# Kernel tuning notes

Measured on AMD Instinct MI355X. Metric: run time of the kernel, lower is better.

## Reference

```python
import jax, jax.numpy as jnp
import numpy as np

B, S, E, H = 4, 2048, 1024, 16
HD = E // H  # head_dim = 64


def setup_inputs() -> dict:
    key = jax.random.key(0)
    ks = jax.random.split(key, 9)
    s_in = 1.0 / np.sqrt(E)
    return {
        "x": jax.random.normal(ks[0], (B, S, E), dtype=jnp.float32),
        "Wq": jax.random.normal(ks[1], (E, E), dtype=jnp.float32) * s_in,
        "bq": jax.random.normal(ks[2], (E,), dtype=jnp.float32) * 0.01,
        "Wk": jax.random.normal(ks[3], (E, E), dtype=jnp.float32) * s_in,
        "bk": jax.random.normal(ks[4], (E,), dtype=jnp.float32) * 0.01,
        "Wv": jax.random.normal(ks[5], (E, E), dtype=jnp.float32) * s_in,
        "bv": jax.random.normal(ks[6], (E,), dtype=jnp.float32) * 0.01,
        "Wo": jax.random.normal(ks[7], (E, E), dtype=jnp.float32) * s_in,
        "bo": jax.random.normal(ks[8], (E,), dtype=jnp.float32) * 0.01,
    }


def reference(x, Wq, bq, Wk, bk, Wv, bv, Wo, bo):
    b, s, e = x.shape
    # fused QKV projections (equivalent to concatenated per-head linears)
    q = x @ Wq + bq  # [b, s, e]
    k = x @ Wk + bk
    v = x @ Wv + bv
    # split heads: [b, h, s, hd]
    def split(t):
        return t.reshape(b, s, H, HD).transpose(0, 2, 1, 3)
    q, k, v = split(q), split(k), split(v)
    scale = 1.0 / np.sqrt(HD)
    attn = jnp.einsum("bhqd,bhkd->bhqk", q, k) * scale  # [b, h, s, s]
    causal = jnp.tril(jnp.ones((s, s), dtype=bool))
    attn = jnp.where(causal[None, None], attn, -jnp.inf)
    attn = jax.nn.softmax(attn, axis=-1)
    y = jnp.einsum("bhqk,bhkd->bhqd", attn, v)  # [b, h, s, hd]
    y = y.transpose(0, 2, 1, 3).reshape(b, s, e)
    return y @ Wo + bo
```

## Files before the change

kernel.cpp:

```cpp
#include <hip/hip_runtime.h>
#include <hip/hip_bf16.h>

#define B_ 4
#define S_ 2048
#define E_ 1024
#define H_ 16
#define HD_ 64
#define QS 3072

typedef __attribute__((ext_vector_type(8))) short bf16x8;
typedef __attribute__((ext_vector_type(4))) float f32x4;

__device__ __forceinline__ float b2f(unsigned short u) {
    union { unsigned u; float f; } v; v.u = ((unsigned)u) << 16; return v.f;
}
__device__ __forceinline__ unsigned short f2b(float f) {
    union { float f; unsigned u; } v; v.f = f;
    unsigned lsb = (v.u >> 16) & 1u;
    v.u += 0x7fffu + lsb;
    return (unsigned short)(v.u >> 16);
}
__device__ __forceinline__ unsigned cvtpk_bf16(float lo, float hi) {
    unsigned r;
    asm("v_cvt_pk_bf16_f32 %0, %1, %2" : "=v"(r) : "v"(lo), "v"(hi));
    return r;
}

typedef const __attribute__((address_space(1))) unsigned glb_u32;
typedef __attribute__((address_space(3))) unsigned lds_u32;
__device__ __forceinline__ void gl_lds16(const unsigned short* g,
                                         unsigned short* l) {
    __builtin_amdgcn_global_load_lds((glb_u32*)g, (lds_u32*)l, 16, 0, 0);
}

__global__ void cvt_f32_to_bf16(const float* __restrict__ in,
                                unsigned short* __restrict__ out, int n8) {
    int i = blockIdx.x * blockDim.x + threadIdx.x;
    if (i >= n8) return;
    const float4* p = (const float4*)(in + (size_t)i * 8);
    float4 a = p[0], b = p[1];
    bf16x8 o;
    o[0] = (short)f2b(a.x); o[1] = (short)f2b(a.y);
    o[2] = (short)f2b(a.z); o[3] = (short)f2b(a.w);
    o[4] = (short)f2b(b.x); o[5] = (short)f2b(b.y);
    o[6] = (short)f2b(b.z); o[7] = (short)f2b(b.w);
    *(bf16x8*)(out + (size_t)i * 8) = o;
}

__global__ void transpose_cvt(const float* __restrict__ W,
                              unsigned short* __restrict__ Wt) {
    __shared__ float tile[32][33];
    int tx = threadIdx.x, ty = threadIdx.y;
    int x0 = blockIdx.x * 32, y0 = blockIdx.y * 32;
#pragma unroll
    for (int j = 0; j < 32; j += 8)
        tile[ty + j][tx] = W[(size_t)(y0 + ty + j) * E_ + x0 + tx];
    __syncthreads();
#pragma unroll
    for (int j = 0; j < 32; j += 8)
        Wt[(size_t)(x0 + ty + j) * E_ + y0 + tx] = f2b(tile[tx][ty + j]);
}

#define BM 128
#define BN 128
#define BK 32

__global__ __launch_bounds__(256) void gemm_bt(
        const unsigned short* __restrict__ A,
        const unsigned short* __restrict__ Bt,
        const float* __restrict__ b0, const float* __restrict__ b1,
        const float* __restrict__ b2,
        unsigned short* __restrict__ Cb,
        int M, int N, int K) {
    __shared__ unsigned short As[BM][BK];
    __shared__ unsigned short Bs[BN][BK];
    int t = threadIdx.x;
    int lane = t & 63, wid = t >> 6;
    int wr = wid >> 1, wc = wid & 1;
    int bx = blockIdx.x, by = blockIdx.y;
    const int row = t >> 2, kc = (t & 3) << 3;
    const unsigned short* ga0 = A + (size_t)(by * BM + row) * K + kc;
    const unsigned short* gb0 = Bt + (size_t)(bx * BN + row) * K + kc;
    unsigned short* la0 = &As[0][0] + (size_t)t * 8;
    unsigned short* lb0 = &Bs[0][0] + (size_t)t * 8;
    const size_t step64 = (size_t)64 * K;

    f32x4 acc[4][4] = {};

    for (int ko = 0; ko < K; ko += BK) {
        gl_lds16(ga0 + ko, la0);
        gl_lds16(ga0 + ko + step64, la0 + 2048);
        gl_lds16(gb0 + ko, lb0);
        gl_lds16(gb0 + ko + step64, lb0 + 2048);
        __syncthreads();
        int kg = (lane >> 4) << 3;
        bf16x8 af[4], bfr[4];
#pragma unroll
        for (int i = 0; i < 4; ++i) {
            af[i]  = *(const bf16x8*)&As[wr * 64 + i * 16 + (lane & 15)][kg];
            bfr[i] = *(const bf16x8*)&Bs[wc * 64 + i * 16 + (lane & 15)][kg];
        }
#pragma unroll
        for (int i = 0; i < 4; ++i)
#pragma unroll
            for (int j = 0; j < 4; ++j)
                acc[i][j] = __builtin_amdgcn_mfma_f32_16x16x32_bf16(
                    af[i], bfr[j], acc[i][j], 0, 0, 0);
        __syncthreads();
    }

#pragma unroll
    for (int i = 0; i < 4; ++i) {
        int row0 = by * BM + wr * 64 + i * 16 + ((lane >> 4) << 2);
#pragma unroll
        for (int j = 0; j < 4; ++j) {
            int col = bx * BN + wc * 64 + j * 16 + (lane & 15);
            const float* bp = (col < 1024) ? b0 : ((col < 2048) ? b1 : b2);
            float bv = bp[col & 1023];
#pragma unroll
            for (int r = 0; r < 4; ++r) {
                int rr = row0 + r;
                Cb[(size_t)rr * N + col] = f2b(acc[i][j][r] + bv);
            }
        }
    }
}

__global__ __launch_bounds__(256) void gemm_bt_out(
        const unsigned short* __restrict__ A,
        const unsigned short* __restrict__ Bt,
        const float* __restrict__ bias,
        float* __restrict__ Cf, int M, int N, int K) {
    __shared__ unsigned short As[64][BK];
    __shared__ unsigned short Bs[BN][BK];
    int t = threadIdx.x;
    int lane = t & 63, wid = t >> 6;
    int wr = wid >> 1, wc = wid & 1;
    int bx = blockIdx.x, by = blockIdx.y;
    const int row = t >> 2, kc = (t & 3) << 3;
    const unsigned short* ga0 = A + (size_t)(by * 64 + row) * K + kc;
    const unsigned short* gb0 = Bt + (size_t)(bx * BN + row) * K + kc;
    unsigned short* la0 = &As[0][0] + (size_t)t * 8;
    unsigned short* lb0 = &Bs[0][0] + (size_t)t * 8;
    const size_t step64 = (size_t)64 * K;

    f32x4 acc[2][4] = {};

    for (int ko = 0; ko < K; ko += BK) {
        gl_lds16(ga0 + ko, la0);
        gl_lds16(gb0 + ko, lb0);
        gl_lds16(gb0 + ko + step64, lb0 + 2048);
        __syncthreads();
        int kg = (lane >> 4) << 3;
        bf16x8 af[2], bfr[4];
#pragma unroll
        for (int i = 0; i < 2; ++i)
            af[i] = *(const bf16x8*)&As[wr * 32 + i * 16 + (lane & 15)][kg];
#pragma unroll
        for (int j = 0; j < 4; ++j)
            bfr[j] = *(const bf16x8*)&Bs[wc * 64 + j * 16 + (lane & 15)][kg];
#pragma unroll
        for (int i = 0; i < 2; ++i)
#pragma unroll
            for (int j = 0; j < 4; ++j)
                acc[i][j] = __builtin_amdgcn_mfma_f32_16x16x32_bf16(
                    af[i], bfr[j], acc[i][j], 0, 0, 0);
        __syncthreads();
    }

#pragma unroll
    for (int i = 0; i < 2; ++i) {
        int row0 = by * 64 + wr * 32 + i * 16 + ((lane >> 4) << 2);
#pragma unroll
        for (int j = 0; j < 4; ++j) {
            int col = bx * BN + wc * 64 + j * 16 + (lane & 15);
            float bv = bias[col];
#pragma unroll
            for (int r = 0; r < 4; ++r)
                Cf[(size_t)(row0 + r) * N + col] = acc[i][j][r] + bv;
        }
    }
}

#define KVBLK 64

__global__ __launch_bounds__(256) void attn_mfma(
        const unsigned short* __restrict__ QKV,
        unsigned short* __restrict__ Yb) {
    __shared__ unsigned short Ks[2][KVBLK][64];
    __shared__ unsigned short Vt[2][64][KVBLK];
    __shared__ unsigned short Pl[4][16][64];

    int t = threadIdx.x;
    int lane = t & 63, wid = t >> 6;
    int l15 = lane & 15, lg = lane >> 4;
    int bh = blockIdx.x;
    int b = bh >> 4, h = bh & 15;
    int by = gridDim.y - 1 - blockIdx.y;
    int qbase = by * 128 + wid * 32;
    int vidx = lg << 4;

    const int kk1 = t >> 3, kk2 = 32 + kk1;
    const int kg1 = ((t & 7) ^ (kk1 & 7)) << 3;
    const int kg2 = ((t & 7) ^ (kk2 & 7)) << 3;
    const int vkey = t >> 2, vc4 = (t & 3) << 4;

    const unsigned short* kvbase = QKV + ((size_t)b * S_) * QS + 1024 + h * 64;

    const float qscale = 0.125f * 1.44269504f;
    bf16x8 qf[2][2];
#pragma unroll
    for (int mt = 0; mt < 2; ++mt)
#pragma unroll
        for (int ks = 0; ks < 2; ++ks) {
            int row = qbase + mt * 16 + l15;
            bf16x8 v = *(const bf16x8*)&QKV[((size_t)(b * S_ + row)) * QS +
                                            h * 64 + ks * 32 + lg * 8];
#pragma unroll
            for (int e = 0; e < 8; ++e)
                qf[mt][ks][e] = (short)f2b(b2f((unsigned short)v[e]) * qscale);
        }

    f32x4 yacc[2][4] = {};
    float m_[2] = {-1e30f, -1e30f}, l_[2] = {0.f, 0.f};

    int ntiles = by * 2 + 2;

    {
        gl_lds16(kvbase + (size_t)kk1 * QS + kg1, &Ks[0][0][0] + (size_t)t * 8);
        gl_lds16(kvbase + (size_t)kk2 * QS + kg2,
                 &Ks[0][0][0] + 2048 + (size_t)t * 8);
        const unsigned short* vsrc = kvbase + 1024 + (size_t)vkey * QS + vc4;
        bf16x8 v0 = *(const bf16x8*)vsrc;
        bf16x8 v1 = *(const bf16x8*)(vsrc + 8);
#pragma unroll
        for (int e = 0; e < 8; ++e) {
            int d0 = vc4 + e, d1 = vc4 + 8 + e;
            int s0 = (d0 & 7) ^ ((d0 >> 3) & 7);
            int s1 = (d1 & 7) ^ ((d1 >> 3) & 7);
            Vt[0][d0][vkey ^ (s0 << 3)] = (unsigned short)v0[e];
            Vt[0][d1][vkey ^ (s1 << 3)] = (unsigned short)v1[e];
        }
    }
    __syncthreads();

    int cur = 0;
    for (int kt = 0; kt < ntiles; ++kt) {
        int k0 = kt * KVBLK;
        bool pre = (kt + 1 < ntiles);
        bf16x8 nv0, nv1;
        if (pre) {
            const unsigned short* kb = kvbase + (size_t)(k0 + KVBLK) * QS;
            unsigned short* ld = &Ks[cur ^ 1][0][0];
            gl_lds16(kb + (size_t)kk1 * QS + kg1, ld + (size_t)t * 8);
            gl_lds16(kb + (size_t)kk2 * QS + kg2, ld + 2048 + (size_t)t * 8);
            const unsigned short* vsrc =
                kb + 1024 + (size_t)vkey * QS + vc4;
            nv0 = *(const bf16x8*)vsrc;
            nv1 = *(const bf16x8*)(vsrc + 8);
        }

        if (k0 <= qbase + 31) {
            bool boundary = (k0 + KVBLK - 1 > qbase);
            f32x4 sacc[2][4] = {};
#pragma unroll
            for (int ks = 0; ks < 2; ++ks) {
                bf16x8 kf[4];
#pragma unroll
                for (int n = 0; n < 4; ++n)
                    kf[n] = *(const bf16x8*)&Ks[cur][n * 16 + l15]
                              [(ks * 32 + lg * 8) ^ ((l15 & 7) << 3)];
#pragma unroll
                for (int mt = 0; mt < 2; ++mt)
#pragma unroll
                    for (int n = 0; n < 4; ++n)
                        sacc[mt][n] = __builtin_amdgcn_mfma_f32_16x16x32_bf16(
                            kf[n], qf[mt][ks], sacc[mt][n], 0, 0, 0);
            }

#pragma unroll
            for (int mt = 0; mt < 2; ++mt) {
                int qv = qbase + mt * 16 + l15;
                if (boundary) {
#pragma unroll
                    for (int n = 0; n < 4; ++n)
#pragma unroll
                        for (int r = 0; r < 4; ++r)
                            if (k0 + n * 16 + lg * 4 + r > qv)
                                sacc[mt][n][r] = -3e38f;
                }
                float pm = -3e38f;
#pragma unroll
                for (int n = 0; n < 4; ++n)
#pragma unroll
                    for (int r = 0; r < 4; ++r)
                        pm = fmaxf(pm, sacc[mt][n][r]);
                pm = fmaxf(pm, __shfl_xor(pm, 16));
                pm = fmaxf(pm, __shfl_xor(pm, 32));
                float mo = m_[mt];
                float mn = mo;
                bool need = __any(pm > mo + 8.0f);
                if (need) {
                    mn = fmaxf(mo, pm);
                    float corr = __builtin_exp2f(mo - mn);
                    m_[mt] = mn;
                    l_[mt] *= corr;
                    int ci = __float_as_int(corr);
#pragma unroll
                    for (int r = 0; r < 4; ++r) {
                        float cq = __int_as_float(
                            __builtin_amdgcn_ds_bpermute(vidx + 4 * r, ci));
#pragma unroll
                        for (int n = 0; n < 4; ++n) yacc[mt][n][r] *= cq;
                    }
                }
                float rs = 0.f;
#pragma unroll
                for (int n = 0; n < 4; ++n)
#pragma unroll
                    for (int r = 0; r < 4; ++r) {
                        float p = __builtin_exp2f(sacc[mt][n][r] - mn);
                        sacc[mt][n][r] = p;
                        rs += p;
                    }
                rs += __shfl_xor(rs, 16);
                rs += __shfl_xor(rs, 32);
                l_[mt] += rs;
#pragma unroll
                for (int n = 0; n < 4; ++n)
#pragma unroll
                    for (int j = 0; j < 2; ++j) {
                        unsigned u = cvtpk_bf16(sacc[mt][n][2 * j],
                                                sacc[mt][n][2 * j + 1]);
                        int col = (n * 16 + lg * 4 + 2 * j) ^ ((l15 & 7) << 3);
                        *(unsigned*)&Pl[wid][l15][col] = u;
                    }
#pragma unroll
                for (int ks = 0; ks < 2; ++ks) {
                    bf16x8 pa, vf[4];
                    pa = *(const bf16x8*)&Pl[wid][l15]
                           [(ks * 32 + lg * 8) ^ ((l15 & 7) << 3)];
#pragma unroll
                    for (int nd = 0; nd < 4; ++nd) {
                        int d = nd * 16 + l15;
                        int sig = (d & 7) ^ ((d >> 3) & 7);
                        vf[nd] = *(const bf16x8*)&Vt[cur][d]
                                   [(ks * 32 + lg * 8) ^ (sig << 3)];
                    }
#pragma unroll
                    for (int nd = 0; nd < 4; ++nd)
                        yacc[mt][nd] = __builtin_amdgcn_mfma_f32_16x16x32_bf16(
                            pa, vf[nd], yacc[mt][nd], 0, 0, 0);
                }
            }
        }

        if (pre) {
#pragma unroll
            for (int e = 0; e < 8; ++e) {
                int d0 = vc4 + e, d1 = vc4 + 8 + e;
                int s0 = (d0 & 7) ^ ((d0 >> 3) & 7);
                int s1 = (d1 & 7) ^ ((d1 >> 3) & 7);
                Vt[cur ^ 1][d0][vkey ^ (s0 << 3)] = (unsigned short)nv0[e];
                Vt[cur ^ 1][d1][vkey ^ (s1 << 3)] = (unsigned short)nv1[e];
            }
        }
        __syncthreads();
        cur ^= 1;
    }

#pragma unroll
    for (int mt = 0; mt < 2; ++mt) {
        float inv = 1.f / l_[mt];
        int ii = __float_as_int(inv);
        float iv[4];
#pragma unroll
        for (int r = 0; r < 4; ++r)
            iv[r] = __int_as_float(
                __builtin_amdgcn_ds_bpermute(vidx + 4 * r, ii));
#pragma unroll
        for (int n = 0; n < 4; ++n)
#pragma unroll
            for (int r = 0; r < 4; ++r) {
                int row = qbase + mt * 16 + lg * 4 + r;
                int d = n * 16 + l15;
                Yb[((size_t)(b * S_ + row)) * E_ + h * 64 + d] =
                    f2b(yacc[mt][n][r] * iv[r]);
            }
    }
}

extern "C" void kernel_launch(void* const* d_in, const int* in_sizes, int n_in,
                              void* d_out, int out_size, void* d_ws, size_t ws_size,
                              hipStream_t stream) {
    const float* x  = (const float*)d_in[0];
    const float* Wq = (const float*)d_in[1];
    const float* bq = (const float*)d_in[2];
    const float* Wk = (const float*)d_in[3];
    const float* bk = (const float*)d_in[4];
    const float* Wv = (const float*)d_in[5];
    const float* bv = (const float*)d_in[6];
    const float* Wo = (const float*)d_in[7];
    const float* bo = (const float*)d_in[8];

    char* ws = (char*)d_ws;
    const size_t M = (size_t)B_ * S_;
    unsigned short* xb   = (unsigned short*)ws;
    unsigned short* QKVb = (unsigned short*)(ws + (16ull << 20));
    unsigned short* Wqkv = (unsigned short*)(ws + (64ull << 20));
    unsigned short* Wto  = (unsigned short*)(ws + (70ull << 20));
    unsigned short* Yb   = xb;

    int n8 = (int)(M * E_ / 8);
    cvt_f32_to_bf16<<<(n8 + 255) / 256, 256, 0, stream>>>(x, xb, n8);

    dim3 tb(32, 8), tg(32, 32);
    transpose_cvt<<<tg, tb, 0, stream>>>(Wq, Wqkv);
    transpose_cvt<<<tg, tb, 0, stream>>>(Wk, Wqkv + (size_t)1024 * E_);
    transpose_cvt<<<tg, tb, 0, stream>>>(Wv, Wqkv + (size_t)2048 * E_);
    transpose_cvt<<<tg, tb, 0, stream>>>(Wo, Wto);

    dim3 gq(QS / BN, M / BM);
    gemm_bt<<<gq, 256, 0, stream>>>(xb, Wqkv, bq, bk, bv, QKVb,
                                    (int)M, QS, E_);

    dim3 ag(B_ * H_, S_ / 128);
    attn_mfma<<<ag, 256, 0, stream>>>(QKVb, Yb);

    dim3 gg(E_ / BN, M / 64);
    gemm_bt_out<<<gg, 256, 0, stream>>>(Yb, Wto, bo, (float*)d_out,
                                        (int)M, E_, E_);
}
```

Baseline: 217.6 us.

## Make attention persistent with atomic work queue and merge weight transposes

The attention kernel becomes persistent: 768 blocks take (query-tile, head) units from a global atomic counter, heaviest causal tiles first, which is meant to improve load balance across CUs. It also adds s_setprio around MFMA sections, hoists the V fragment loads ahead of the softmax, and defers the cross-lane row-sum reduction to the end of the loop. The four weight transpose launches are merged into a single 3D-grid launch. In exchange it adds a memset launch and an atomic per work unit, and the launch-bounds occupancy hint of 3 may add register pressure.

```diff
diff --git a/kernel.cpp b/kernel.cpp
--- a/kernel.cpp
+++ b/kernel.cpp
@@ -7,6 +7,7 @@
 #define H_ 16
 #define HD_ 64
 #define QS 3072
+#define NUNITS (B_ * H_ * (S_ / 128))
 
 typedef __attribute__((ext_vector_type(8))) short bf16x8;
 typedef __attribute__((ext_vector_type(4))) float f32x4;
@@ -47,9 +48,16 @@
     *(bf16x8*)(out + (size_t)i * 8) = o;
 }
 
-__global__ void transpose_cvt(const float* __restrict__ W,
-                              unsigned short* __restrict__ Wt) {
+__global__ void transpose_cvt4(const float* __restrict__ W0,
+                               const float* __restrict__ W1,
+                               const float* __restrict__ W2,
+                               const float* __restrict__ W3,
+                               unsigned short* __restrict__ Wqkv,
+                               unsigned short* __restrict__ Wto) {
     __shared__ float tile[32][33];
+    int z = blockIdx.z;
+    const float* W = (z == 0) ? W0 : (z == 1) ? W1 : (z == 2) ? W2 : W3;
+    unsigned short* Wt = (z < 3) ? Wqkv + (size_t)z * 1024 * E_ : Wto;
     int tx = threadIdx.x, ty = threadIdx.y;
     int x0 = blockIdx.x * 32, y0 = blockIdx.y * 32;
 #pragma unroll
@@ -184,209 +192,233 @@
 
 #define KVBLK 64
 
-__global__ __launch_bounds__(256) void attn_mfma(
+__global__ __launch_bounds__(256, 3) void attn_mfma(
         const unsigned short* __restrict__ QKV,
-        unsigned short* __restrict__ Yb) {
+        unsigned short* __restrict__ Yb,
+        unsigned int* __restrict__ counter) {
     __shared__ unsigned short Ks[2][KVBLK][64];
     __shared__ unsigned short Vt[2][64][KVBLK];
     __shared__ unsigned short Pl[4][16][64];
+    __shared__ unsigned int s_u;
 
     int t = threadIdx.x;
     int lane = t & 63, wid = t >> 6;
     int l15 = lane & 15, lg = lane >> 4;
-    int bh = blockIdx.x;
-    int b = bh >> 4, h = bh & 15;
-    int by = gridDim.y - 1 - blockIdx.y;
-    int qbase = by * 128 + wid * 32;
     int vidx = lg << 4;
 
     const int kk1 = t >> 3, kk2 = 32 + kk1;
     const int kg1 = ((t & 7) ^ (kk1 & 7)) << 3;
     const int kg2 = ((t & 7) ^ (kk2 & 7)) << 3;
     const int vkey = t >> 2, vc4 = (t & 3) << 4;
-
-    const unsigned short* kvbase = QKV + ((size_t)b * S_) * QS + 1024 + h * 64;
-
     const float qscale = 0.125f * 1.44269504f;
-    bf16x8 qf[2][2];
-#pragma unroll
-    for (int mt = 0; mt < 2; ++mt)
-#pragma unroll
-        for (int ks = 0; ks < 2; ++ks) {
-            int row = qbase + mt * 16 + l15;
-            bf16x8 v = *(const bf16x8*)&QKV[((size_t)(b * S_ + row)) * QS +
-                                            h * 64 + ks * 32 + lg * 8];
-#pragma unroll
-            for (int e = 0; e < 8; ++e)
-                qf[mt][ks][e] = (short)f2b(b2f((unsigned short)v[e]) * qscale);
-        }
-
-    f32x4 yacc[2][4] = {};
-    float m_[2] = {-1e30f, -1e30f}, l_[2] = {0.f, 0.f};
-
-    int ntiles = by * 2 + 2;
-
-    {
-        gl_lds16(kvbase + (size_t)kk1 * QS + kg1, &Ks[0][0][0] + (size_t)t * 8);
-        gl_lds16(kvbase + (size_t)kk2 * QS + kg2,
-                 &Ks[0][0][0] + 2048 + (size_t)t * 8);
-        const unsigned short* vsrc = kvbase + 1024 + (size_t)vkey * QS + vc4;
-        bf16x8 v0 = *(const bf16x8*)vsrc;
-        bf16x8 v1 = *(const bf16x8*)(vsrc + 8);
-#pragma unroll
-        for (int e = 0; e < 8; ++e) {
-            int d0 = vc4 + e, d1 = vc4 + 8 + e;
-            int s0 = (d0 & 7) ^ ((d0 >> 3) & 7);
-            int s1 = (d1 & 7) ^ ((d1 >> 3) & 7);
-            Vt[0][d0][vkey ^ (s0 << 3)] = (unsigned short)v0[e];
-            Vt[0][d1][vkey ^ (s1 << 3)] = (unsigned short)v1[e];
-        }
-    }
-    __syncthreads();
-
-    int cur = 0;
-    for (int kt = 0; kt < ntiles; ++kt) {
-        int k0 = kt * KVBLK;
-        bool pre = (kt + 1 < ntiles);
-        bf16x8 nv0, nv1;
-        if (pre) {
-            const unsigned short* kb = kvbase + (size_t)(k0 + KVBLK) * QS;
-            unsigned short* ld = &Ks[cur ^ 1][0][0];
-            gl_lds16(kb + (size_t)kk1 * QS + kg1, ld + (size_t)t * 8);
-            gl_lds16(kb + (size_t)kk2 * QS + kg2, ld + 2048 + (size_t)t * 8);
+
+    for (;;) {
+        __syncthreads();
+        if (t == 0) s_u = atomicAdd(counter, 1u);
+        __syncthreads();
+        unsigned u = s_u;
+        if (u >= (unsigned)NUNITS) break;
+        int qt = (S_ / 128 - 1) - (int)(u >> 6);
+        int bh = (int)(u & 63);
+        int b = bh >> 4, h = bh & 15;
+        int qbase = qt * 128 + wid * 32;
+        const unsigned short* kvbase =
+            QKV + ((size_t)b * S_) * QS + 1024 + h * 64;
+
+        bf16x8 qf[2][2];
+#pragma unroll
+        for (int mt = 0; mt < 2; ++mt)
+#pragma unroll
+            for (int ks = 0; ks < 2; ++ks) {
+                int row = qbase + mt * 16 + l15;
+                bf16x8 v = *(const bf16x8*)&QKV[((size_t)(b * S_ + row)) * QS +
+                                                h * 64 + ks * 32 + lg * 8];
+#pragma unroll
+                for (int e = 0; e < 8; ++e)
+                    qf[mt][ks][e] =
+                        (short)f2b(b2f((unsigned short)v[e]) * qscale);
+            }
+
+        f32x4 yacc[2][4] = {};
+        float m_[2] = {-1e30f, -1e30f}, l_[2] = {0.f, 0.f};
+        int ntiles = qt * 2 + 2;
+
+        {
+            gl_lds16(kvbase + (size_t)kk1 * QS + kg1,
+                     &Ks[0][0][0] + (size_t)t * 8);
+            gl_lds16(kvbase + (size_t)kk2 * QS + kg2,
+                     &Ks[0][0][0] + 2048 + (size_t)t * 8);
             const unsigned short* vsrc =
-                kb + 1024 + (size_t)vkey * QS + vc4;
-            nv0 = *(const bf16x8*)vsrc;
-            nv1 = *(const bf16x8*)(vsrc + 8);
-        }
-
-        if (k0 <= qbase + 31) {
-            bool boundary = (k0 + KVBLK - 1 > qbase);
-            f32x4 sacc[2][4] = {};
-#pragma unroll
-            for (int ks = 0; ks < 2; ++ks) {
-                bf16x8 kf[4];
-#pragma unroll
-                for (int n = 0; n < 4; ++n)
-                    kf[n] = *(const bf16x8*)&Ks[cur][n * 16 + l15]
-                              [(ks * 32 + lg * 8) ^ ((l15 & 7) << 3)];
-#pragma unroll
-                for (int mt = 0; mt < 2; ++mt)
-#pragma unroll
-                    for (int n = 0; n < 4; ++n)
-                        sacc[mt][n] = __builtin_amdgcn_mfma_f32_16x16x32_bf16(
-                            kf[n], qf[mt][ks], sacc[mt][n], 0, 0, 0);
-            }
-
-#pragma unroll
-            for (int mt = 0; mt < 2; ++mt) {
-                int qv = qbase + mt * 16 + l15;
-                if (boundary) {
-#pragma unroll
-                    for (int n = 0; n < 4; ++n)
-#pragma unroll
-                        for (int r = 0; r < 4; ++r)
-                            if (k0 + n * 16 + lg * 4 + r > qv)
-                                sacc[mt][n][r] = -3e38f;
-                }
-                float pm = -3e38f;
-#pragma unroll
-                for (int n = 0; n < 4; ++n)
-#pragma unroll
-                    for (int r = 0; r < 4; ++r)
-                        pm = fmaxf(pm, sacc[mt][n][r]);
-                pm = fmaxf(pm, __shfl_xor(pm, 16));
-                pm = fmaxf(pm, __shfl_xor(pm, 32));
-                float mo = m_[mt];
-                float mn = mo;
-                bool need = __any(pm > mo + 8.0f);
-                if (need) {
-                    mn = fmaxf(mo, pm);
-                    float corr = __builtin_exp2f(mo - mn);
-                    m_[mt] = mn;
-                    l_[mt] *= corr;
-                    int ci = __float_as_int(corr);
-#pragma unroll
-                    for (int r = 0; r < 4; ++r) {
-                        float cq = __int_as_float(
-                            __builtin_amdgcn_ds_bpermute(vidx + 4 * r, ci));
-#pragma unroll
-                        for (int n = 0; n < 4; ++n) yacc[mt][n][r] *= cq;
-                    }
-                }
-                float rs = 0.f;
-#pragma unroll
-                for (int n = 0; n < 4; ++n)
-#pragma unroll
-                    for (int r = 0; r < 4; ++r) {
-                        float p = __builtin_exp2f(sacc[mt][n][r] - mn);
-                        sacc[mt][n][r] = p;
-                        rs += p;
-                    }
-                rs += __shfl_xor(rs, 16);
-                rs += __shfl_xor(rs, 32);
-                l_[mt] += rs;
-#pragma unroll
-                for (int n = 0; n < 4; ++n)
-#pragma unroll
-                    for (int j = 0; j < 2; ++j) {
-                        unsigned u = cvtpk_bf16(sacc[mt][n][2 * j],
-                                                sacc[mt][n][2 * j + 1]);
-                        int col = (n * 16 + lg * 4 + 2 * j) ^ ((l15 & 7) << 3);
-                        *(unsigned*)&Pl[wid][l15][col] = u;
-                    }
-#pragma unroll
-                for (int ks = 0; ks < 2; ++ks) {
-                    bf16x8 pa, vf[4];
-                    pa = *(const bf16x8*)&Pl[wid][l15]
-                           [(ks * 32 + lg * 8) ^ ((l15 & 7) << 3)];
-#pragma unroll
-                    for (int nd = 0; nd < 4; ++nd) {
-                        int d = nd * 16 + l15;
-                        int sig = (d & 7) ^ ((d >> 3) & 7);
-                        vf[nd] = *(const bf16x8*)&Vt[cur][d]
-                                   [(ks * 32 + lg * 8) ^ (sig << 3)];
-                    }
-#pragma unroll
-                    for (int nd = 0; nd < 4; ++nd)
-                        yacc[mt][nd] = __builtin_amdgcn_mfma_f32_16x16x32_bf16(
-                            pa, vf[nd], yacc[mt][nd], 0, 0, 0);
-                }
-            }
-        }
-
-        if (pre) {
+                kvbase + 1024 + (size_t)vkey * QS + vc4;
+            bf16x8 v0 = *(const bf16x8*)vsrc;
+            bf16x8 v1 = *(const bf16x8*)(vsrc + 8);
 #pragma unroll
             for (int e = 0; e < 8; ++e) {
                 int d0 = vc4 + e, d1 = vc4 + 8 + e;
                 int s0 = (d0 & 7) ^ ((d0 >> 3) & 7);
                 int s1 = (d1 & 7) ^ ((d1 >> 3) & 7);
-                Vt[cur ^ 1][d0][vkey ^ (s0 << 3)] = (unsigned short)nv0[e];
-                Vt[cur ^ 1][d1][vkey ^ (s1 << 3)] = (unsigned short)nv1[e];
-            }
-        }
-        __syncthreads();
-        cur ^= 1;
-    }
-
-#pragma unroll
-    for (int mt = 0; mt < 2; ++mt) {
-        float inv = 1.f / l_[mt];
-        int ii = __float_as_int(inv);
-        float iv[4];
-#pragma unroll
-        for (int r = 0; r < 4; ++r)
-            iv[r] = __int_as_float(
-                __builtin_amdgcn_ds_bpermute(vidx + 4 * r, ii));
-#pragma unroll
-        for (int n = 0; n < 4; ++n)
-#pragma unroll
-            for (int r = 0; r < 4; ++r) {
-                int row = qbase + mt * 16 + lg * 4 + r;
-                int d = n * 16 + l15;
-                Yb[((size_t)(b * S_ + row)) * E_ + h * 64 + d] =
-                    f2b(yacc[mt][n][r] * iv[r]);
-            }
+                Vt[0][d0][vkey ^ (s0 << 3)] = (unsigned short)v0[e];
+                Vt[0][d1][vkey ^ (s1 << 3)] = (unsigned short)v1[e];
+            }
+        }
+        __syncthreads();
+
+        int cur = 0;
+        for (int kt = 0; kt < ntiles; ++kt) {
+            int k0 = kt * KVBLK;
+            bool pre = (kt + 1 < ntiles);
+            bf16x8 nv0, nv1;
+            if (pre) {
+                const unsigned short* kb = kvbase + (size_t)(k0 + KVBLK) * QS;
+                unsigned short* ld = &Ks[cur ^ 1][0][0];
+                gl_lds16(kb + (size_t)kk1 * QS + kg1, ld + (size_t)t * 8);
+                gl_lds16(kb + (size_t)kk2 * QS + kg2,
+                         ld + 2048 + (size_t)t * 8);
+                const unsigned short* vsrc =
+                    kb + 1024 + (size_t)vkey * QS + vc4;
+                nv0 = *(const bf16x8*)vsrc;
+                nv1 = *(const bf16x8*)(vsrc + 8);
+            }
+
+            if (k0 <= qbase + 31) {
+                bool boundary = (k0 + KVBLK - 1 > qbase);
+                f32x4 sacc[2][4] = {};
+                __builtin_amdgcn_s_setprio(1);
+#pragma unroll
+                for (int ks = 0; ks < 2; ++ks) {
+                    bf16x8 kf[4];
+#pragma unroll
+                    for (int n = 0; n < 4; ++n)
+                        kf[n] = *(const bf16x8*)&Ks[cur][n * 16 + l15]
+                                  [(ks * 32 + lg * 8) ^ ((l15 & 7) << 3)];
+#pragma unroll
+                    for (int mt = 0; mt < 2; ++mt)
+#pragma unroll
+                        for (int n = 0; n < 4; ++n)
+                            sacc[mt][n] =
+                                __builtin_amdgcn_mfma_f32_16x16x32_bf16(
+                                    kf[n], qf[mt][ks], sacc[mt][n], 0, 0, 0);
+                }
+                __builtin_amdgcn_s_setprio(0);
+
+                bf16x8 vf[2][4];
+#pragma unroll
+                for (int ks = 0; ks < 2; ++ks)
+#pragma unroll
+                    for (int nd = 0; nd < 4; ++nd) {
+                        int d = nd * 16 + l15;
+                        int sig = (d & 7) ^ ((d >> 3) & 7);
+                        vf[ks][nd] = *(const bf16x8*)&Vt[cur][d]
+                                       [(ks * 32 + lg * 8) ^ (sig << 3)];
+                    }
+
+#pragma unroll
+                for (int mt = 0; mt < 2; ++mt) {
+                    int qv = qbase + mt * 16 + l15;
+                    if (boundary) {
+#pragma unroll
+                        for (int n = 0; n < 4; ++n)
+#pragma unroll
+                            for (int r = 0; r < 4; ++r)
+                                if (k0 + n * 16 + lg * 4 + r > qv)
+                                    sacc[mt][n][r] = -3e38f;
+                    }
+                    float pm = -3e38f;
+#pragma unroll
+                    for (int n = 0; n < 4; ++n)
+#pragma unroll
+                        for (int r = 0; r < 4; ++r)
+                            pm = fmaxf(pm, sacc[mt][n][r]);
+                    pm = fmaxf(pm, __shfl_xor(pm, 16));
+                    pm = fmaxf(pm, __shfl_xor(pm, 32));
+                    float mo = m_[mt];
+                    float mn = mo;
+                    bool need = __any(pm > mo + 8.0f);
+                    if (need) {
+                        mn = fmaxf(mo, pm);
+                        float corr = __builtin_exp2f(mo - mn);
+                        m_[mt] = mn;
+                        l_[mt] *= corr;
+                        int ci = __float_as_int(corr);
+#pragma unroll
+                        for (int r = 0; r < 4; ++r) {
+                            float cq = __int_as_float(
+                                __builtin_amdgcn_ds_bpermute(vidx + 4 * r, ci));
+#pragma unroll
+                            for (int n = 0; n < 4; ++n) yacc[mt][n][r] *= cq;
+                        }
+                    }
+                    float rs = 0.f;
+#pragma unroll
+                    for (int n = 0; n < 4; ++n)
+#pragma unroll
+                        for (int r = 0; r < 4; ++r) {
+                            float p = __builtin_exp2f(sacc[mt][n][r] - mn);
+                            sacc[mt][n][r] = p;
+                            rs += p;
+                        }
+                    l_[mt] += rs;
+#pragma unroll
+                    for (int n = 0; n < 4; ++n)
+#pragma unroll
+                        for (int j = 0; j < 2; ++j) {
+                            unsigned pu = cvtpk_bf16(sacc[mt][n][2 * j],
+                                                     sacc[mt][n][2 * j + 1]);
+                            int col = (n * 16 + lg * 4 + 2 * j) ^
+                                      ((l15 & 7) << 3);
+                            *(unsigned*)&Pl[wid][l15][col] = pu;
+                        }
+                    __builtin_amdgcn_s_setprio(1);
+#pragma unroll
+                    for (int ks = 0; ks < 2; ++ks) {
+                        bf16x8 pa = *(const bf16x8*)&Pl[wid][l15]
+                                      [(ks * 32 + lg * 8) ^ ((l15 & 7) << 3)];
+#pragma unroll
+                        for (int nd = 0; nd < 4; ++nd)
+                            yacc[mt][nd] =
+                                __builtin_amdgcn_mfma_f32_16x16x32_bf16(
+                                    pa, vf[ks][nd], yacc[mt][nd], 0, 0, 0);
+                    }
+                    __builtin_amdgcn_s_setprio(0);
+                }
+            }
+
+            if (pre) {
+#pragma unroll
+                for (int e = 0; e < 8; ++e) {
+                    int d0 = vc4 + e, d1 = vc4 + 8 + e;
+                    int s0 = (d0 & 7) ^ ((d0 >> 3) & 7);
+                    int s1 = (d1 & 7) ^ ((d1 >> 3) & 7);
+                    Vt[cur ^ 1][d0][vkey ^ (s0 << 3)] = (unsigned short)nv0[e];
+                    Vt[cur ^ 1][d1][vkey ^ (s1 << 3)] = (unsigned short)nv1[e];
+                }
+            }
+            __syncthreads();
+            cur ^= 1;
+        }
+
+#pragma unroll
+        for (int mt = 0; mt < 2; ++mt) {
+            float lt = l_[mt];
+            lt += __shfl_xor(lt, 16);
+            lt += __shfl_xor(lt, 32);
+            float inv = 1.f / lt;
+            int ii = __float_as_int(inv);
+            float iv[4];
+#pragma unroll
+            for (int r = 0; r < 4; ++r)
+                iv[r] = __int_as_float(
+                    __builtin_amdgcn_ds_bpermute(vidx + 4 * r, ii));
+#pragma unroll
+            for (int n = 0; n < 4; ++n)
+#pragma unroll
+                for (int r = 0; r < 4; ++r) {
+                    int row = qbase + mt * 16 + lg * 4 + r;
+                    int d = n * 16 + l15;
+                    Yb[((size_t)(b * S_ + row)) * E_ + h * 64 + d] =
+                        f2b(yacc[mt][n][r] * iv[r]);
+                }
+        }
     }
 }
 
@@ -409,23 +441,21 @@
     unsigned short* QKVb = (unsigned short*)(ws + (16ull << 20));
     unsigned short* Wqkv = (unsigned short*)(ws + (64ull << 20));
     unsigned short* Wto  = (unsigned short*)(ws + (70ull << 20));
+    unsigned int*   cnt  = (unsigned int*)(ws + (72ull << 20));
     unsigned short* Yb   = xb;
 
     int n8 = (int)(M * E_ / 8);
     cvt_f32_to_bf16<<<(n8 + 255) / 256, 256, 0, stream>>>(x, xb, n8);
 
-    dim3 tb(32, 8), tg(32, 32);
-    transpose_cvt<<<tg, tb, 0, stream>>>(Wq, Wqkv);
-    transpose_cvt<<<tg, tb, 0, stream>>>(Wk, Wqkv + (size_t)1024 * E_);
-    transpose_cvt<<<tg, tb, 0, stream>>>(Wv, Wqkv + (size_t)2048 * E_);
-    transpose_cvt<<<tg, tb, 0, stream>>>(Wo, Wto);
+    dim3 tb(32, 8), tg(32, 32, 4);
+    transpose_cvt4<<<tg, tb, 0, stream>>>(Wq, Wk, Wv, Wo, Wqkv, Wto);
 
     dim3 gq(QS / BN, M / BM);
     gemm_bt<<<gq, 256, 0, stream>>>(xb, Wqkv, bq, bk, bv, QKVb,
                                     (int)M, QS, E_);
 
-    dim3 ag(B_ * H_, S_ / 128);
-    attn_mfma<<<ag, 256, 0, stream>>>(QKVb, Yb);
+    hipMemsetAsync(cnt, 0, sizeof(unsigned), stream);
+    attn_mfma<<<768, 256, 0, stream>>>(QKVb, Yb, cnt);
 
     dim3 gg(E_ / BN, M / 64);
     gemm_bt_out<<<gg, 256, 0, stream>>>(Yb, Wto, bo, (float*)d_out,
```

Measured after the change: 266.3 us. 22.4% more time.

## Merge weight transposes, add setprio around MFMAs, defer row-sum reduction

Applied to the files above, without the earlier changes.

Folds the four weight transpose-convert launches into one launch that uses blockIdx.z to pick the matrix. In the attention kernel it adds s_setprio around the MFMA blocks and sets a launch-bounds occupancy hint of 4. It also moves the cross-lane shuffle reduction of the softmax row sum out of the KV loop so it runs once at the end. These cut launch overhead and per-tile shuffle work and aim to improve wave scheduling, at the cost of possible register pressure from the occupancy hint.

```diff
diff --git a/kernel.cpp b/kernel.cpp
--- a/kernel.cpp
+++ b/kernel.cpp
@@ -47,9 +47,16 @@
     *(bf16x8*)(out + (size_t)i * 8) = o;
 }
 
-__global__ void transpose_cvt(const float* __restrict__ W,
-                              unsigned short* __restrict__ Wt) {
+__global__ void transpose_cvt4(const float* __restrict__ W0,
+                               const float* __restrict__ W1,
+                               const float* __restrict__ W2,
+                               const float* __restrict__ W3,
+                               unsigned short* __restrict__ Wqkv,
+                               unsigned short* __restrict__ Wto) {
     __shared__ float tile[32][33];
+    int z = blockIdx.z;
+    const float* W = (z == 0) ? W0 : (z == 1) ? W1 : (z == 2) ? W2 : W3;
+    unsigned short* Wt = (z < 3) ? Wqkv + (size_t)z * 1024 * E_ : Wto;
     int tx = threadIdx.x, ty = threadIdx.y;
     int x0 = blockIdx.x * 32, y0 = blockIdx.y * 32;
 #pragma unroll
@@ -184,7 +191,7 @@
 
 #define KVBLK 64
 
-__global__ __launch_bounds__(256) void attn_mfma(
+__global__ __launch_bounds__(256, 4) void attn_mfma(
         const unsigned short* __restrict__ QKV,
         unsigned short* __restrict__ Yb) {
     __shared__ unsigned short Ks[2][KVBLK][64];
@@ -263,6 +270,7 @@
         if (k0 <= qbase + 31) {
             bool boundary = (k0 + KVBLK - 1 > qbase);
             f32x4 sacc[2][4] = {};
+            __builtin_amdgcn_s_setprio(1);
 #pragma unroll
             for (int ks = 0; ks < 2; ++ks) {
                 bf16x8 kf[4];
@@ -277,6 +285,7 @@
                         sacc[mt][n] = __builtin_amdgcn_mfma_f32_16x16x32_bf16(
                             kf[n], qf[mt][ks], sacc[mt][n], 0, 0, 0);
             }
+            __builtin_amdgcn_s_setprio(0);
 
 #pragma unroll
             for (int mt = 0; mt < 2; ++mt) {
@@ -323,8 +332,6 @@
                         sacc[mt][n][r] = p;
                         rs += p;
                     }
-                rs += __shfl_xor(rs, 16);
-                rs += __shfl_xor(rs, 32);
                 l_[mt] += rs;
 #pragma unroll
                 for (int n = 0; n < 4; ++n)
@@ -335,6 +342,7 @@
                         int col = (n * 16 + lg * 4 + 2 * j) ^ ((l15 & 7) << 3);
                         *(unsigned*)&Pl[wid][l15][col] = u;
                     }
+                __builtin_amdgcn_s_setprio(1);
 #pragma unroll
                 for (int ks = 0; ks < 2; ++ks) {
                     bf16x8 pa, vf[4];
@@ -352,6 +360,7 @@
                         yacc[mt][nd] = __builtin_amdgcn_mfma_f32_16x16x32_bf16(
                             pa, vf[nd], yacc[mt][nd], 0, 0, 0);
                 }
+                __builtin_amdgcn_s_setprio(0);
             }
         }
 
@@ -371,7 +380,10 @@
 
 #pragma unroll
     for (int mt = 0; mt < 2; ++mt) {
-        float inv = 1.f / l_[mt];
+        float lt = l_[mt];
+        lt += __shfl_xor(lt, 16);
+        lt += __shfl_xor(lt, 32);
+        float inv = 1.f / lt;
         int ii = __float_as_int(inv);
         float iv[4];
 #pragma unroll
@@ -414,11 +426,8 @@
     int n8 = (int)(M * E_ / 8);
     cvt_f32_to_bf16<<<(n8 + 255) / 256, 256, 0, stream>>>(x, xb, n8);
 
-    dim3 tb(32, 8), tg(32, 32);
-    transpose_cvt<<<tg, tb, 0, stream>>>(Wq, Wqkv);
-    transpose_cvt<<<tg, tb, 0, stream>>>(Wk, Wqkv + (size_t)1024 * E_);
-    transpose_cvt<<<tg, tb, 0, stream>>>(Wv, Wqkv + (size_t)2048 * E_);
-    transpose_cvt<<<tg, tb, 0, stream>>>(Wo, Wto);
+    dim3 tb(32, 8), tg(32, 32, 4);
+    transpose_cvt4<<<tg, tb, 0, stream>>>(Wq, Wk, Wv, Wo, Wqkv, Wto);
 
     dim3 gq(QS / BN, M / BM);
     gemm_bt<<<gq, 256, 0, stream>>>(xb, Wqkv, bq, bk, bv, QKVb,
```

After: 327.4 us. 1.5x slower.
